# Optimization experiments

Hardware: AMD Instinct MI355X
Metric: run time of the kernel (lower is better)

The kernel has to match this reference:

```python
import jax, jax.numpy as jnp
import numpy as np

THRESHOLD = 1.5  # IF neuron fires when a + b > 1.5, i.e. both bits are 1


def setup_inputs() -> dict:
    key = jax.random.key(0)
    # Binary bit inputs in {0.0, 1.0}, shape [batch, n_bits]
    bits = jax.random.randint(key, (65536, 1024), 0, 2)
    return {"x": bits.astype(jnp.float32)}


def reference(x) -> jnp.ndarray:
    """Parallel AND-tree over the last dim: returns [..., 1], 1.0 iff all bits are 1.

    Each level pairs adjacent elements, sums them, and applies the IF-neuron
    spiking threshold (V = a + b > 1.5 -> spike). Odd-length levels carry the
    last element through unchanged, exactly as in the torch module.
    Shapes are static at trace time, so the Python while-loop is jit-safe.
    """
    current = x
    while current.shape[-1] > 1:
        n = current.shape[-1]
        if n % 2 == 1:
            pairs = current[..., :-1]
            last = current[..., -1:]
        else:
            pairs = current
            last = None
        # Fused pairwise add + threshold (VecAND gate)
        spk = (pairs[..., 0::2] + pairs[..., 1::2] > THRESHOLD).astype(current.dtype)
        current = spk if last is None else jnp.concatenate([spk, last], axis=-1)
    return current
```

## Files before the change

### kernel.cpp

```cpp
#include <hip/hip_runtime.h>


#define COLS 1024
#define WAVES_PER_BLOCK 4

__global__ __launch_bounds__(256) void VecANDTree_43860206027289_kernel(
    const float* __restrict__ x, float* __restrict__ out, int rows) {
    const int lane = threadIdx.x & 63;
    const int row = blockIdx.x * WAVES_PER_BLOCK + (threadIdx.x >> 6);
    if (row >= rows) return;

    const float* rp = x + (size_t)row * COLS;

    bool ok = rp[lane] > 0.5f;
    if (__builtin_expect(!__all(ok), 1)) {
        if (lane == 0) out[row] = 0.0f;
        return;
    }

    float r = 1.0f;
#pragma unroll 1
    for (int c = 1; c < COLS / 64; ++c) {
        ok = rp[c * 64 + lane] > 0.5f;
        if (!__all(ok)) { r = 0.0f; break; }
    }
    if (lane == 0) out[row] = r;
}

extern "C" void kernel_launch(void* const* d_in, const int* in_sizes, int n_in,
                              void* d_out, int out_size, void* d_ws, size_t ws_size,
                              hipStream_t stream) {
    const float* x = (const float*)d_in[0];
    float* out = (float*)d_out;
    const int rows = out_size;
    const int blocks = (rows + WAVES_PER_BLOCK - 1) / WAVES_PER_BLOCK;
    VecANDTree_43860206027289_kernel<<<blocks, 256, 0, stream>>>(x, out, rows);
}
```

Measured before the change: 295.4 us.

## Batch 32 rows per wave with 16-column probes before full row scan

Each wave now handles 32 rows. Each lane loads a 16-column prefix from 8 different rows up front, and one ballot per load checks 4 rows at once. Only rows whose prefix is all ones fall back to a full 1024-column scan. This cuts bytes fetched per row and raises memory-level parallelism in the latency-bound early-exit kernel. The cost is a serialized fallback path when many rows pass the probe.

Measured after the change: 292.2 us. Within noise of the previous version (-1.1%).

```diff
diff --git a/kernel.cpp b/kernel.cpp
--- a/kernel.cpp
+++ b/kernel.cpp
@@ -2,29 +2,54 @@
 
 
 #define COLS 1024
-#define WAVES_PER_BLOCK 4
+#define ROWS_PER_WAVE 32
+#define LOADS_PER_WAVE (ROWS_PER_WAVE / 4)
+#define THREADS 256
+#define WAVES_PER_BLOCK (THREADS / 64)
 
-__global__ __launch_bounds__(256) void VecANDTree_43860206027289_kernel(
+__device__ __forceinline__ float full_row_scan(const float* __restrict__ rp,
+                                               int lane) {
+#pragma unroll 1
+    for (int c = 0; c < COLS / 64; ++c) {
+        if (!__all(rp[c * 64 + lane] > 0.5f)) return 0.0f;
+    }
+    return 1.0f;
+}
+
+__global__ __launch_bounds__(THREADS) void VecANDTree_43860206027289_kernel(
     const float* __restrict__ x, float* __restrict__ out, int rows) {
     const int lane = threadIdx.x & 63;
-    const int row = blockIdx.x * WAVES_PER_BLOCK + (threadIdx.x >> 6);
-    if (row >= rows) return;
+    const int wave = blockIdx.x * WAVES_PER_BLOCK + (threadIdx.x >> 6);
+    const int base = wave * ROWS_PER_WAVE;
+    if (base >= rows) return;
 
-    const float* rp = x + (size_t)row * COLS;
+    const int sub = lane >> 4;
+    const int col = lane & 15;
+    const size_t lane_off = (size_t)sub * COLS + col;
+    const float* bp = x + (size_t)base * COLS + lane_off;
 
-    bool ok = rp[lane] > 0.5f;
-    if (__builtin_expect(!__all(ok), 1)) {
-        if (lane == 0) out[row] = 0.0f;
-        return;
+    float v[LOADS_PER_WAVE];
+#pragma unroll
+    for (int l = 0; l < LOADS_PER_WAVE; ++l) {
+        v[l] = bp[(size_t)l * 4 * COLS];
     }
 
-    float r = 1.0f;
-#pragma unroll 1
-    for (int c = 1; c < COLS / 64; ++c) {
-        ok = rp[c * 64 + lane] > 0.5f;
-        if (!__all(ok)) { r = 0.0f; break; }
+    float res = 0.0f;
+#pragma unroll
+    for (int l = 0; l < LOADS_PER_WAVE; ++l) {
+        const unsigned long long m = __ballot(v[l] > 0.5f);
+#pragma unroll
+        for (int g = 0; g < 4; ++g) {
+            const bool pass = ((m >> (16 * g)) & 0xFFFFull) == 0xFFFFull;
+            float r = 0.0f;
+            if (pass) {
+                r = full_row_scan(x + (size_t)(base + 4 * l + g) * COLS, lane);
+            }
+            if (lane == 4 * l + g) res = r;
+        }
     }
-    if (lane == 0) out[row] = r;
+
+    if (lane < ROWS_PER_WAVE) out[base + lane] = res;
 }
 
 extern "C" void kernel_launch(void* const* d_in, const int* in_sizes, int n_in,
@@ -33,6 +58,7 @@
     const float* x = (const float*)d_in[0];
     float* out = (float*)d_out;
     const int rows = out_size;
-    const int blocks = (rows + WAVES_PER_BLOCK - 1) / WAVES_PER_BLOCK;
-    VecANDTree_43860206027289_kernel<<<blocks, 256, 0, stream>>>(x, out, rows);
+    const int waves = (rows + ROWS_PER_WAVE - 1) / ROWS_PER_WAVE;
+    const int blocks = (waves + WAVES_PER_BLOCK - 1) / WAVES_PER_BLOCK;
+    VecANDTree_43860206027289_kernel<<<blocks, THREADS, 0, stream>>>(x, out, rows);
 }
```
